# Optimization experiments

Hardware: AMD Instinct MI355X
Metric: run time of the kernel (lower is better)

Reference implementation:

```python
import jax, jax.numpy as jnp
import numpy as np

# dims matching init_kwargs / input_specs
N, C, H, W = 8, 256, 64, 64
OUT_C, KH, KW = 256, 3, 3
STRIDE, PAD = 1, 1
OUT_H = (H - KH + 2 * PAD) // STRIDE + 1  # 64
OUT_W = (W - KW + 2 * PAD) // STRIDE + 1  # 64
K = KH * KW


def setup_inputs() -> dict:
    key = jax.random.key(0)
    k1, k2, k3 = jax.random.split(key, 3)
    x = jax.random.normal(k1, (N, C, H, W), dtype=jnp.float32)
    offset = jax.random.normal(k2, (N, 2 * K, OUT_H, OUT_W), dtype=jnp.float32)
    # kaiming-uniform-ish scale for weight (fan_in = C*KH*KW)
    bound = 1.0 / np.sqrt(C * KH * KW)
    weight = jax.random.uniform(k3, (OUT_C, C, KH, KW), dtype=jnp.float32,
                                minval=-bound, maxval=bound)
    return {"input": x, "offset": offset, "weight": weight}


def _deform_conv(x, offset, weight):
    # base sampling positions in pixel coords: y = oy*stride + ky - pad
    ky = jnp.repeat(jnp.arange(KH, dtype=jnp.float32) - PAD, KW)  # [K]
    kx = jnp.tile(jnp.arange(KW, dtype=jnp.float32) - PAD, KH)    # [K]
    oy = jnp.arange(OUT_H, dtype=jnp.float32) * STRIDE            # [outH]
    ox = jnp.arange(OUT_W, dtype=jnp.float32) * STRIDE            # [outW]
    base_y = ky[:, None, None] + oy[None, :, None]  # [K, outH, 1]
    base_x = kx[:, None, None] + ox[None, None, :]  # [K, 1, outW]

    off = offset.reshape(N, K, 2, OUT_H, OUT_W)
    y = base_y[None] + off[:, :, 0]  # [N, K, outH, outW], offset channel 0 = dy
    xp = base_x[None] + off[:, :, 1]  # channel 1 = dx

    # bilinear sample with zero padding (grid_sample align_corners=True, zeros)
    y0 = jnp.floor(y)
    x0 = jnp.floor(xp)
    bidx = jnp.arange(N)[:, None, None, None]
    acc = jnp.zeros((N, K, OUT_H, OUT_W, C), dtype=x.dtype)
    for dy in (0.0, 1.0):
        for dx in (0.0, 1.0):
            yi = y0 + dy
            xi = x0 + dx
            wgt = (1.0 - jnp.abs(y - yi)) * (1.0 - jnp.abs(xp - xi))
            valid = ((yi >= 0) & (yi <= H - 1) & (xi >= 0) & (xi <= W - 1))
            yc = jnp.clip(yi, 0, H - 1).astype(jnp.int32)
            xc = jnp.clip(xi, 0, W - 1).astype(jnp.int32)
            g = x[bidx, :, yc, xc]  # [N, K, outH, outW, C]
            acc = acc + g * (wgt * valid.astype(x.dtype))[..., None]

    # weight.view(outC, -1) flattens (C, KH, KW) -> (C, K) ordering
    w = weight.reshape(OUT_C, C, K)
    out = jnp.einsum('nkhwc,ock->nohw', acc, w)  # [N, outC, outH, outW]
    return out


def reference(input, offset, weight):
    # NOTE: original forward never adds bias -> faithfully omitted
    return _deform_conv(input, offset, weight)
```

## Files before the change

### kernel.cpp

```cpp
#include <hip/hip_runtime.h>
#include <hip/hip_fp16.h>
#include <stdint.h>


typedef _Float16 half8 __attribute__((ext_vector_type(8)));
typedef float f32x4 __attribute__((ext_vector_type(4)));

__device__ __forceinline__ __half2 h2(uint32_t u) {
  return __builtin_bit_cast(__half2, u);
}
__device__ __forceinline__ uint32_t packh2f(float a, float b) {
  return __builtin_bit_cast(uint32_t, __floats2half2_rn(a, b));
}
__device__ __forceinline__ __half2 duplo(uint32_t u) {
  return __half2half2(__builtin_bit_cast(__half, (unsigned short)(u & 0xffffu)));
}
__device__ __forceinline__ __half2 duphi(uint32_t u) {
  return __half2half2(__builtin_bit_cast(__half, (unsigned short)(u >> 16)));
}

__global__ __launch_bounds__(256) void prep_all_kernel(
    const float* __restrict__ x, const float* __restrict__ w,
    const float* __restrict__ offset,
    unsigned short* __restrict__ xb, unsigned short* __restrict__ w3s,
    unsigned short* __restrict__ coords) {
  __shared__ float tile[64][65];
  int tid = threadIdx.x;
  if (blockIdx.x < 2048) {
    int bn   = blockIdx.x >> 8;
    int rem  = blockIdx.x & 255;
    int y    = rem >> 2;
    int cblk = rem & 3;
    const float* src = x + ((size_t)(bn * 256 + cblk * 64)) * 4096 + y * 64;
#pragma unroll
    for (int i = 0; i < 4; ++i) {
      int u  = i * 256 + tid;
      int cl = u >> 4;
      int xs = (u & 15) * 4;
      float4 v = *(const float4*)(src + cl * 4096 + xs);
      tile[cl][xs] = v.x; tile[cl][xs + 1] = v.y;
      tile[cl][xs + 2] = v.z; tile[cl][xs + 3] = v.w;
    }
    __syncthreads();
    unsigned short* dst = xb + ((size_t)(bn * 64 + y) * 64) * 256 + cblk * 64;
#pragma unroll
    for (int i = 0; i < 8; ++i) {
      int v2  = i * 256 + tid;
      int xc  = v2 >> 5;
      int cl2 = (v2 & 31) * 2;
      *(uint32_t*)(dst + xc * 256 + cl2) = packh2f(tile[cl2][xc], tile[cl2 + 1][xc]);
    }
  } else if (blockIdx.x < 4352) {
    int idx = (blockIdx.x - 2048) * 256 + tid;
    int t   = idx >> 14;
    int r2  = idx & 16383;
    int g   = r2 >> 3;
    int e   = r2 & 7;
    int oc  = g >> 3;
    int kk8 = (g & 7) ^ (oc & 7);
    int kk  = kk8 * 8 + e;
    int c   = (t & 3) * 64 + kk;
    int k   = t >> 2;
    w3s[idx] = __builtin_bit_cast(unsigned short, __float2half(w[(oc * 256 + c) * 9 + k]));
  } else {
    int idx = (blockIdx.x - 4352) * 256 + tid;
    int ow  = idx & 63;
    int oh  = (idx >> 6) & 63;
    int r   = idx >> 12;
    int k   = r % 9;
    int bn  = r / 9;
    int ky = k / 3 - 1;
    int kx = k % 3 - 1;
    float offy = offset[((bn * 18 + 2 * k    ) * 64 + oh) * 64 + ow];
    float offx = offset[((bn * 18 + 2 * k + 1) * 64 + oh) * 64 + ow];
    float y = (float)(oh + ky) + offy;
    float x2 = (float)(ow + kx) + offx;
    float y0f = floorf(y), x0f = floorf(x2);
    float fy = y - y0f, fx = x2 - x0f;
    int y0 = (int)y0f, x0 = (int)x0f;
    int y1 = y0 + 1, x1 = x0 + 1;
    float vy0 = (y0 >= 0 && y0 <= 63) ? 1.0f : 0.0f;
    float vy1 = (y1 >= 0 && y1 <= 63) ? 1.0f : 0.0f;
    float vx0 = (x0 >= 0 && x0 <= 63) ? 1.0f : 0.0f;
    float vx1 = (x1 >= 0 && x1 <= 63) ? 1.0f : 0.0f;
    float wy0 = (1.0f - fy) * vy0, wy1 = fy * vy1;
    float wx0 = (1.0f - fx) * vx0, wx1 = fx * vx1;
    int y0c = min(max(y0, 0), 63), y1c = min(max(y1, 0), 63);
    int x0c = min(max(x0, 0), 63), x1c = min(max(x1, 0), 63);
    unsigned short ent[8];
    ent[0] = __builtin_bit_cast(unsigned short, __float2half(wy0 * wx0));
    ent[1] = __builtin_bit_cast(unsigned short, __float2half(wy0 * wx1));
    ent[2] = __builtin_bit_cast(unsigned short, __float2half(wy1 * wx0));
    ent[3] = __builtin_bit_cast(unsigned short, __float2half(wy1 * wx1));
    ent[4] = (unsigned short)(y0c * 64 + x0c);
    ent[5] = (unsigned short)(y0c * 64 + x1c);
    ent[6] = (unsigned short)(y1c * 64 + x0c);
    ent[7] = (unsigned short)(y1c * 64 + x1c);
    *(uint4*)(coords + (size_t)idx * 8) = *(const uint4*)ent;
  }
}

__global__ __launch_bounds__(512, 4) void deform_mfma_kernel(
    const unsigned short* __restrict__ xb,
    const unsigned short* __restrict__ coords,
    const unsigned short* __restrict__ w3s,
    float* __restrict__ out) {
  __shared__ __align__(16) unsigned short At[64 * 72];
  __shared__ __align__(16) unsigned short Bt[256 * 64];

  int bn  = blockIdx.x & 7;
  int oh  = blockIdx.x >> 3;
  int tid = threadIdx.x;

  int w    = tid >> 6;
  int lane = tid & 63;
  int wrow = w & 1;
  int wcol = w >> 1;
  int mrow = lane & 15;
  int quad = lane >> 4;

  int srow = tid >> 3;
  int sg   = tid & 7;

  const unsigned short* xbn = xb + (size_t)bn * (64 * 64 * 256);
  const char* gbase = (const char*)xbn + sg * 16;
  const unsigned short* cbase = coords + ((size_t)((bn * 9) * 64 + oh) * 64 + srow) * 8;
  unsigned short* awr = At + srow * 72 + sg * 8;

  f32x4 acc[2][4] = {};

#define BDMA(TT)                                                                \
  {                                                                             \
    const unsigned short* src = w3s + (TT) * 16384;                             \
    _Pragma("unroll")                                                           \
    for (int j = 0; j < 4; ++j) {                                               \
      int base16 = j * 512 + w * 64;                                            \
      __builtin_amdgcn_global_load_lds(                                         \
          (const __attribute__((address_space(1))) void*)(src + (base16 + lane) * 8), \
          (__attribute__((address_space(3))) void*)(Bt + base16 * 8),           \
          16, 0, 0);                                                            \
    }                                                                           \
  }

#define ASTAGE(TT)                                                              \
  {                                                                             \
    uint4 c00 = *(const uint4*)(p00 + ((TT) & 3) * 128);                        \
    uint4 c01 = *(const uint4*)(p01 + ((TT) & 3) * 128);                        \
    uint4 c10 = *(const uint4*)(p10 + ((TT) & 3) * 128);                        \
    uint4 c11 = *(const uint4*)(p11 + ((TT) & 3) * 128);                        \
    __half2 r0 = __hmul2(h2(c00.x), w00);                                       \
    r0 = __hfma2(h2(c01.x), w01, r0);                                           \
    r0 = __hfma2(h2(c10.x), w10, r0);                                           \
    r0 = __hfma2(h2(c11.x), w11, r0);                                           \
    __half2 r1 = __hmul2(h2(c00.y), w00);                                       \
    r1 = __hfma2(h2(c01.y), w01, r1);                                           \
    r1 = __hfma2(h2(c10.y), w10, r1);                                           \
    r1 = __hfma2(h2(c11.y), w11, r1);                                           \
    __half2 r2 = __hmul2(h2(c00.z), w00);                                       \
    r2 = __hfma2(h2(c01.z), w01, r2);                                           \
    r2 = __hfma2(h2(c10.z), w10, r2);                                           \
    r2 = __hfma2(h2(c11.z), w11, r2);                                           \
    __half2 r3 = __hmul2(h2(c00.w), w00);                                       \
    r3 = __hfma2(h2(c01.w), w01, r3);                                           \
    r3 = __hfma2(h2(c10.w), w10, r3);                                           \
    r3 = __hfma2(h2(c11.w), w11, r3);                                           \
    uint4 pk;                                                                   \
    pk.x = __builtin_bit_cast(uint32_t, r0);                                    \
    pk.y = __builtin_bit_cast(uint32_t, r1);                                    \
    pk.z = __builtin_bit_cast(uint32_t, r2);                                    \
    pk.w = __builtin_bit_cast(uint32_t, r3);                                    \
    *(uint4*)awr = pk;                                                          \
  }

#define TAPSETUP(TAP)                                                           \
  {                                                                             \
    uint4 ce = *(const uint4*)(cbase + (TAP) * 32768);                          \
    w00 = duplo(ce.x); w01 = duphi(ce.x);                                       \
    w10 = duplo(ce.y); w11 = duphi(ce.y);                                       \
    p00 = gbase + ((size_t)(ce.z & 0xffffu) << 9);                              \
    p01 = gbase + ((size_t)(ce.z >> 16) << 9);                                  \
    p10 = gbase + ((size_t)(ce.w & 0xffffu) << 9);                              \
    p11 = gbase + ((size_t)(ce.w >> 16) << 9);                                  \
  }

  __half2 w00, w01, w10, w11;
  const char *p00, *p01, *p10, *p11;

  TAPSETUP(0)
  BDMA(0)
  ASTAGE(0)
  __syncthreads();

  half8 af[2][2];
  half8 bfr[2][4];

  for (int tap = 0; tap < 9; ++tap) {
#pragma unroll
    for (int cc = 0; cc < 4; ++cc) {
      const int t = tap * 4 + cc;
#pragma unroll
      for (int ks = 0; ks < 2; ++ks) {
#pragma unroll
        for (int m = 0; m < 2; ++m)
          af[m][ks] = *(const half8*)(&At[(wrow * 32 + m * 16 + mrow) * 72 + ks * 32 + quad * 8]);
#pragma unroll
        for (int nn = 0; nn < 4; ++nn) {
          int oc  = wcol * 64 + nn * 16 + mrow;
          int g16 = oc * 8 + ((ks * 4 + quad) ^ (mrow & 7));
          bfr[ks][nn] = *(const half8*)(&Bt[g16 * 8]);
        }
      }
      __syncthreads();

      if (t < 35) {
        BDMA(t + 1)
        if (cc == 3) TAPSETUP(tap + 1)
        ASTAGE(t + 1)
      }
#pragma unroll
      for (int ks = 0; ks < 2; ++ks)
#pragma unroll
        for (int m = 0; m < 2; ++m)
#pragma unroll
          for (int nn = 0; nn < 4; ++nn)
            acc[m][nn] = __builtin_amdgcn_mfma_f32_16x16x32_f16(af[m][ks], bfr[ks][nn], acc[m][nn], 0, 0, 0);
      __syncthreads();
    }
  }

  float* outp = out + (size_t)(bn * 256) * 4096 + oh * 64;
#pragma unroll
  for (int m = 0; m < 2; ++m) {
    int ow0 = wrow * 32 + m * 16 + quad * 4;
#pragma unroll
    for (int nn = 0; nn < 4; ++nn) {
      int oc = wcol * 64 + nn * 16 + mrow;
      *(f32x4*)(outp + oc * 4096 + ow0) = acc[m][nn];
    }
  }
#undef BDMA
#undef ASTAGE
#undef TAPSETUP
}

extern "C" void kernel_launch(void* const* d_in, const int* in_sizes, int n_in,
                              void* d_out, int out_size, void* d_ws, size_t ws_size,
                              hipStream_t stream) {
  (void)in_sizes; (void)n_in; (void)out_size; (void)ws_size;
  const float* x      = (const float*)d_in[0];
  const float* offset = (const float*)d_in[1];
  const float* weight = (const float*)d_in[2];
  float* out = (float*)d_out;

  unsigned short* xb     = (unsigned short*)d_ws;
  unsigned short* w3s    = xb + (size_t)8 * 64 * 64 * 256;
  unsigned short* coords = w3s + (size_t)36 * 16384;

  prep_all_kernel<<<5504, 256, 0, stream>>>(x, weight, offset, xb, w3s, coords);
  deform_mfma_kernel<<<512, 512, 0, stream>>>(xb, coords, w3s, out);
}
```

Baseline: 152.2 us.

## Double-buffer LDS A/B tiles and drop one barrier per k-step

Both the gathered-input tile and the weight tile in shared memory now have two buffers. The next stage's DMA and bilinear gather write into the other buffer while MFMA fragments are read from the current one, so one of the two __syncthreads per step goes away. The A tile drops its padded stride in favour of an XOR swizzle, and the coordinate entry for the next tap is fetched one stage ahead. The cost is roughly double the LDS footprint, which may reduce how many blocks fit on a CU.

```diff
diff --git a/kernel.cpp b/kernel.cpp
--- a/kernel.cpp
+++ b/kernel.cpp
@@ -105,8 +105,8 @@
     const unsigned short* __restrict__ coords,
     const unsigned short* __restrict__ w3s,
     float* __restrict__ out) {
-  __shared__ __align__(16) unsigned short At[64 * 72];
-  __shared__ __align__(16) unsigned short Bt[256 * 64];
+  __shared__ __align__(16) unsigned short At[2][64 * 64];
+  __shared__ __align__(16) unsigned short Bt[2][256 * 64];
 
   int bn  = blockIdx.x & 7;
   int oh  = blockIdx.x >> 3;
@@ -125,11 +125,13 @@
   const unsigned short* xbn = xb + (size_t)bn * (64 * 64 * 256);
   const char* gbase = (const char*)xbn + sg * 16;
   const unsigned short* cbase = coords + ((size_t)((bn * 9) * 64 + oh) * 64 + srow) * 8;
-  unsigned short* awr = At + srow * 72 + sg * 8;
+  int aw_off = srow * 64 + ((sg ^ (srow & 7)) * 8);
+  unsigned short* awr0 = &At[0][0] + aw_off;
+  unsigned short* awr1 = &At[1][0] + aw_off;
 
   f32x4 acc[2][4] = {};
 
-#define BDMA(TT)                                                                \
+#define BDMA(TT, BB)                                                            \
   {                                                                             \
     const unsigned short* src = w3s + (TT) * 16384;                             \
     _Pragma("unroll")                                                           \
@@ -137,12 +139,12 @@
       int base16 = j * 512 + w * 64;                                            \
       __builtin_amdgcn_global_load_lds(                                         \
           (const __attribute__((address_space(1))) void*)(src + (base16 + lane) * 8), \
-          (__attribute__((address_space(3))) void*)(Bt + base16 * 8),           \
+          (__attribute__((address_space(3))) void*)(&Bt[BB][0] + base16 * 8),   \
           16, 0, 0);                                                            \
     }                                                                           \
   }
 
-#define ASTAGE(TT)                                                              \
+#define ASTAGE(TT, AW)                                                          \
   {                                                                             \
     uint4 c00 = *(const uint4*)(p00 + ((TT) & 3) * 128);                        \
     uint4 c01 = *(const uint4*)(p01 + ((TT) & 3) * 128);                        \
@@ -169,26 +171,29 @@
     pk.y = __builtin_bit_cast(uint32_t, r1);                                    \
     pk.z = __builtin_bit_cast(uint32_t, r2);                                    \
     pk.w = __builtin_bit_cast(uint32_t, r3);                                    \
-    *(uint4*)awr = pk;                                                          \
-  }
-
-#define TAPSETUP(TAP)                                                           \
+    *(uint4*)(AW) = pk;                                                         \
+  }
+
+#define TAPSETUP_R(CE)                                                          \
   {                                                                             \
-    uint4 ce = *(const uint4*)(cbase + (TAP) * 32768);                          \
-    w00 = duplo(ce.x); w01 = duphi(ce.x);                                       \
-    w10 = duplo(ce.y); w11 = duphi(ce.y);                                       \
-    p00 = gbase + ((size_t)(ce.z & 0xffffu) << 9);                              \
-    p01 = gbase + ((size_t)(ce.z >> 16) << 9);                                  \
-    p10 = gbase + ((size_t)(ce.w & 0xffffu) << 9);                              \
-    p11 = gbase + ((size_t)(ce.w >> 16) << 9);                                  \
+    w00 = duplo((CE).x); w01 = duphi((CE).x);                                   \
+    w10 = duplo((CE).y); w11 = duphi((CE).y);                                   \
+    p00 = gbase + ((size_t)((CE).z & 0xffffu) << 9);                            \
+    p01 = gbase + ((size_t)((CE).z >> 16) << 9);                                \
+    p10 = gbase + ((size_t)((CE).w & 0xffffu) << 9);                            \
+    p11 = gbase + ((size_t)((CE).w >> 16) << 9);                                \
   }
 
   __half2 w00, w01, w10, w11;
   const char *p00, *p01, *p10, *p11;
-
-  TAPSETUP(0)
-  BDMA(0)
-  ASTAGE(0)
+  uint4 cnext;
+
+  {
+    uint4 ce0 = *(const uint4*)(cbase);
+    TAPSETUP_R(ce0)
+  }
+  BDMA(0, 0)
+  ASTAGE(0, awr0)
   __syncthreads();
 
   half8 af[2][2];
@@ -197,26 +202,35 @@
   for (int tap = 0; tap < 9; ++tap) {
 #pragma unroll
     for (int cc = 0; cc < 4; ++cc) {
-      const int t = tap * 4 + cc;
-#pragma unroll
-      for (int ks = 0; ks < 2; ++ks) {
-#pragma unroll
-        for (int m = 0; m < 2; ++m)
-          af[m][ks] = *(const half8*)(&At[(wrow * 32 + m * 16 + mrow) * 72 + ks * 32 + quad * 8]);
-#pragma unroll
-        for (int nn = 0; nn < 4; ++nn) {
-          int oc  = wcol * 64 + nn * 16 + mrow;
-          int g16 = oc * 8 + ((ks * 4 + quad) ^ (mrow & 7));
-          bfr[ks][nn] = *(const half8*)(&Bt[g16 * 8]);
+      const int t  = tap * 4 + cc;
+      const int pb = cc & 1;
+
+      if (t < 35) {
+        BDMA(t + 1, 1 - pb)
+        if (cc == 2 && tap < 8) cnext = *(const uint4*)(cbase + (tap + 1) * 32768);
+        if (cc == 3) TAPSETUP_R(cnext)
+        ASTAGE(t + 1, pb ? awr0 : awr1)
+      }
+
+      {
+        const unsigned short* Atp = &At[pb][0];
+        const unsigned short* Btp = &Bt[pb][0];
+#pragma unroll
+        for (int ks = 0; ks < 2; ++ks) {
+#pragma unroll
+          for (int m = 0; m < 2; ++m) {
+            int R = wrow * 32 + m * 16 + mrow;
+            af[m][ks] = *(const half8*)(Atp + R * 64 + (((ks * 4 + quad) ^ (mrow & 7)) * 8));
+          }
+#pragma unroll
+          for (int nn = 0; nn < 4; ++nn) {
+            int oc  = wcol * 64 + nn * 16 + mrow;
+            int g16 = oc * 8 + ((ks * 4 + quad) ^ (mrow & 7));
+            bfr[ks][nn] = *(const half8*)(Btp + g16 * 8);
+          }
         }
       }
-      __syncthreads();
-
-      if (t < 35) {
-        BDMA(t + 1)
-        if (cc == 3) TAPSETUP(tap + 1)
-        ASTAGE(t + 1)
-      }
+
 #pragma unroll
       for (int ks = 0; ks < 2; ++ks)
 #pragma unroll
@@ -224,6 +238,7 @@
 #pragma unroll
           for (int nn = 0; nn < 4; ++nn)
             acc[m][nn] = __builtin_amdgcn_mfma_f32_16x16x32_f16(af[m][ks], bfr[ks][nn], acc[m][nn], 0, 0, 0);
+
       __syncthreads();
     }
   }
@@ -240,7 +255,7 @@
   }
 #undef BDMA
 #undef ASTAGE
-#undef TAPSETUP
+#undef TAPSETUP_R
 }
 
 extern "C" void kernel_launch(void* const* d_in, const int* in_sizes, int n_in,
```

Result: faster. 147.1 us (-3.3%).

## Process two output rows per block with register-held weights and double-buffered LDS

Applied to the files above, without the earlier changes.

Each block now computes two output rows (128 pixels × 256 oc), halving the grid, so each wave covers 64 pixels × 64 oc with a 4×4 accumulator tile. Weight fragments are loaded straight from global memory into registers (alternating two register sets) instead of being staged in LDS with global_load_lds. The A tile is double-buffered in an XOR-swizzled LDS layout, so each stage needs one barrier instead of two. This raises register pressure (launch bounds drop to 2 blocks/CU) and puts repeated weight reads on the global/L2 path in exchange for more MFMA reuse per loaded fragment.

```diff
diff --git a/kernel.cpp b/kernel.cpp
--- a/kernel.cpp
+++ b/kernel.cpp
@@ -100,16 +100,15 @@
   }
 }
 
-__global__ __launch_bounds__(512, 4) void deform_mfma_kernel(
+__global__ __launch_bounds__(512, 2) void deform_mfma_kernel(
     const unsigned short* __restrict__ xb,
     const unsigned short* __restrict__ coords,
     const unsigned short* __restrict__ w3s,
     float* __restrict__ out) {
-  __shared__ __align__(16) unsigned short At[64 * 72];
-  __shared__ __align__(16) unsigned short Bt[256 * 64];
+  __shared__ __align__(16) unsigned short At[2][128 * 64];
 
   int bn  = blockIdx.x & 7;
-  int oh  = blockIdx.x >> 3;
+  int ohp = blockIdx.x >> 3;
   int tid = threadIdx.x;
 
   int w    = tid >> 6;
@@ -122,125 +121,158 @@
   int srow = tid >> 3;
   int sg   = tid & 7;
 
-  const unsigned short* xbn = xb + (size_t)bn * (64 * 64 * 256);
-  const char* gbase = (const char*)xbn + sg * 16;
-  const unsigned short* cbase = coords + ((size_t)((bn * 9) * 64 + oh) * 64 + srow) * 8;
-  unsigned short* awr = At + srow * 72 + sg * 8;
-
-  f32x4 acc[2][4] = {};
-
-#define BDMA(TT)                                                                \
-  {                                                                             \
-    const unsigned short* src = w3s + (TT) * 16384;                             \
+  const char* xbc = (const char*)(xb + (size_t)bn * (64 * 64 * 256));
+  const unsigned short* cb0 = coords + ((size_t)((bn * 9) * 64 + ohp * 2) * 64 + srow) * 8;
+  const unsigned short* cb1 = cb0 + 512;
+
+  int aw0 = srow * 64 + ((sg ^ (srow & 7)) * 8);
+  int grp0 = quad ^ (mrow & 7);
+  int grp1 = (4 + quad) ^ (mrow & 7);
+  int a_off0 = (wrow * 64 + mrow) * 64 + grp0 * 8;
+  int a_off1 = (wrow * 64 + mrow) * 64 + grp1 * 8;
+  int boff0 = ((wcol * 64 + mrow) * 8 + grp0) * 16;
+  int boff1 = ((wcol * 64 + mrow) * 8 + grp1) * 16;
+
+  f32x4 acc[4][4] = {};
+  half8 bA[2][4], bB[2][4];
+
+  __half2 w00, w01, w02, w03, w10, w11, w12, w13;
+  uint32_t o00, o01, o02, o03, o10, o11, o12, o13;
+  uint4 cn0, cn1;
+
+#define BLOADR(TT, BS)                                                          \
+  {                                                                             \
+    const char* wp = (const char*)w3s + (size_t)(TT) * 32768;                   \
     _Pragma("unroll")                                                           \
-    for (int j = 0; j < 4; ++j) {                                               \
-      int base16 = j * 512 + w * 64;                                            \
-      __builtin_amdgcn_global_load_lds(                                         \
-          (const __attribute__((address_space(1))) void*)(src + (base16 + lane) * 8), \
-          (__attribute__((address_space(3))) void*)(Bt + base16 * 8),           \
-          16, 0, 0);                                                            \
-    }                                                                           \
-  }
-
-#define ASTAGE(TT)                                                              \
-  {                                                                             \
-    uint4 c00 = *(const uint4*)(p00 + ((TT) & 3) * 128);                        \
-    uint4 c01 = *(const uint4*)(p01 + ((TT) & 3) * 128);                        \
-    uint4 c10 = *(const uint4*)(p10 + ((TT) & 3) * 128);                        \
-    uint4 c11 = *(const uint4*)(p11 + ((TT) & 3) * 128);                        \
-    __half2 r0 = __hmul2(h2(c00.x), w00);                                       \
-    r0 = __hfma2(h2(c01.x), w01, r0);                                           \
-    r0 = __hfma2(h2(c10.x), w10, r0);                                           \
-    r0 = __hfma2(h2(c11.x), w11, r0);                                           \
-    __half2 r1 = __hmul2(h2(c00.y), w00);                                       \
-    r1 = __hfma2(h2(c01.y), w01, r1);                                           \
-    r1 = __hfma2(h2(c10.y), w10, r1);                                           \
-    r1 = __hfma2(h2(c11.y), w11, r1);                                           \
-    __half2 r2 = __hmul2(h2(c00.z), w00);                                       \
-    r2 = __hfma2(h2(c01.z), w01, r2);                                           \
-    r2 = __hfma2(h2(c10.z), w10, r2);                                           \
-    r2 = __hfma2(h2(c11.z), w11, r2);                                           \
-    __half2 r3 = __hmul2(h2(c00.w), w00);                                       \
-    r3 = __hfma2(h2(c01.w), w01, r3);                                           \
-    r3 = __hfma2(h2(c10.w), w10, r3);                                           \
-    r3 = __hfma2(h2(c11.w), w11, r3);                                           \
-    uint4 pk;                                                                   \
-    pk.x = __builtin_bit_cast(uint32_t, r0);                                    \
-    pk.y = __builtin_bit_cast(uint32_t, r1);                                    \
-    pk.z = __builtin_bit_cast(uint32_t, r2);                                    \
-    pk.w = __builtin_bit_cast(uint32_t, r3);                                    \
-    *(uint4*)awr = pk;                                                          \
-  }
-
-#define TAPSETUP(TAP)                                                           \
-  {                                                                             \
-    uint4 ce = *(const uint4*)(cbase + (TAP) * 32768);                          \
-    w00 = duplo(ce.x); w01 = duphi(ce.x);                                       \
-    w10 = duplo(ce.y); w11 = duphi(ce.y);                                       \
-    p00 = gbase + ((size_t)(ce.z & 0xffffu) << 9);                              \
-    p01 = gbase + ((size_t)(ce.z >> 16) << 9);                                  \
-    p10 = gbase + ((size_t)(ce.w & 0xffffu) << 9);                              \
-    p11 = gbase + ((size_t)(ce.w >> 16) << 9);                                  \
-  }
-
-  __half2 w00, w01, w10, w11;
-  const char *p00, *p01, *p10, *p11;
-
-  TAPSETUP(0)
-  BDMA(0)
-  ASTAGE(0)
+    for (int nn = 0; nn < 4; ++nn) {                                            \
+      BS[0][nn] = *(const half8*)(wp + boff0 + nn * 2048);                      \
+      BS[1][nn] = *(const half8*)(wp + boff1 + nn * 2048);                      \
+    }                                                                           \
+  }
+
+#define TAPSETUP_R(CE0, CE1)                                                    \
+  {                                                                             \
+    w00 = duplo((CE0).x); w01 = duphi((CE0).x);                                 \
+    w02 = duplo((CE0).y); w03 = duphi((CE0).y);                                 \
+    o00 = (((CE0).z & 0xffffu) << 9) + sg * 16;                                 \
+    o01 = (((CE0).z >> 16) << 9) + sg * 16;                                     \
+    o02 = (((CE0).w & 0xffffu) << 9) + sg * 16;                                 \
+    o03 = (((CE0).w >> 16) << 9) + sg * 16;                                     \
+    w10 = duplo((CE1).x); w11 = duphi((CE1).x);                                 \
+    w12 = duplo((CE1).y); w13 = duphi((CE1).y);                                 \
+    o10 = (((CE1).z & 0xffffu) << 9) + sg * 16;                                 \
+    o11 = (((CE1).z >> 16) << 9) + sg * 16;                                     \
+    o12 = (((CE1).w & 0xffffu) << 9) + sg * 16;                                 \
+    o13 = (((CE1).w >> 16) << 9) + sg * 16;                                     \
+  }
+
+#define ASTAGE(TT, ATP)                                                         \
+  {                                                                             \
+    {                                                                           \
+      uint4 c0 = *(const uint4*)(xbc + o00 + ((TT) & 3) * 128);                 \
+      uint4 c1 = *(const uint4*)(xbc + o01 + ((TT) & 3) * 128);                 \
+      uint4 c2 = *(const uint4*)(xbc + o02 + ((TT) & 3) * 128);                 \
+      uint4 c3 = *(const uint4*)(xbc + o03 + ((TT) & 3) * 128);                 \
+      __half2 r0 = __hmul2(h2(c0.x), w00);                                      \
+      r0 = __hfma2(h2(c1.x), w01, r0); r0 = __hfma2(h2(c2.x), w02, r0);         \
+      r0 = __hfma2(h2(c3.x), w03, r0);                                          \
+      __half2 r1 = __hmul2(h2(c0.y), w00);                                      \
+      r1 = __hfma2(h2(c1.y), w01, r1); r1 = __hfma2(h2(c2.y), w02, r1);         \
+      r1 = __hfma2(h2(c3.y), w03, r1);                                          \
+      __half2 r2 = __hmul2(h2(c0.z), w00);                                      \
+      r2 = __hfma2(h2(c1.z), w01, r2); r2 = __hfma2(h2(c2.z), w02, r2);         \
+      r2 = __hfma2(h2(c3.z), w03, r2);                                          \
+      __half2 r3 = __hmul2(h2(c0.w), w00);                                      \
+      r3 = __hfma2(h2(c1.w), w01, r3); r3 = __hfma2(h2(c2.w), w02, r3);         \
+      r3 = __hfma2(h2(c3.w), w03, r3);                                          \
+      uint4 pk;                                                                 \
+      pk.x = __builtin_bit_cast(uint32_t, r0);                                  \
+      pk.y = __builtin_bit_cast(uint32_t, r1);                                  \
+      pk.z = __builtin_bit_cast(uint32_t, r2);                                  \
+      pk.w = __builtin_bit_cast(uint32_t, r3);                                  \
+      *(uint4*)((ATP) + aw0) = pk;                                              \
+    }                                                                           \
+    {                                                                           \
+      uint4 c0 = *(const uint4*)(xbc + o10 + ((TT) & 3) * 128);                 \
+      uint4 c1 = *(const uint4*)(xbc + o11 + ((TT) & 3) * 128);                 \
+      uint4 c2 = *(const uint4*)(xbc + o12 + ((TT) & 3) * 128);                 \
+      uint4 c3 = *(const uint4*)(xbc + o13 + ((TT) & 3) * 128);                 \
+      __half2 r0 = __hmul2(h2(c0.x), w10);                                      \
+      r0 = __hfma2(h2(c1.x), w11, r0); r0 = __hfma2(h2(c2.x), w12, r0);         \
+      r0 = __hfma2(h2(c3.x), w13, r0);                                          \
+      __half2 r1 = __hmul2(h2(c0.y), w10);                                      \
+      r1 = __hfma2(h2(c1.y), w11, r1); r1 = __hfma2(h2(c2.y), w12, r1);         \
+      r1 = __hfma2(h2(c3.y), w13, r1);                                          \
+      __half2 r2 = __hmul2(h2(c0.z), w10);                                      \
+      r2 = __hfma2(h2(c1.z), w11, r2); r2 = __hfma2(h2(c2.z), w12, r2);         \
+      r2 = __hfma2(h2(c3.z), w13, r2);                                          \
+      __half2 r3 = __hmul2(h2(c0.w), w10);                                      \
+      r3 = __hfma2(h2(c1.w), w11, r3); r3 = __hfma2(h2(c2.w), w12, r3);         \
+      r3 = __hfma2(h2(c3.w), w13, r3);                                          \
+      uint4 pk;                                                                 \
+      pk.x = __builtin_bit_cast(uint32_t, r0);                                  \
+      pk.y = __builtin_bit_cast(uint32_t, r1);                                  \
+      pk.z = __builtin_bit_cast(uint32_t, r2);                                  \
+      pk.w = __builtin_bit_cast(uint32_t, r3);                                  \
+      *(uint4*)((ATP) + aw0 + 4096) = pk;                                       \
+    }                                                                           \
+  }
+
+#define COMPUTE(ATP, BS)                                                        \
+  {                                                                             \
+    _Pragma("unroll")                                                           \
+    for (int m = 0; m < 4; ++m) {                                               \
+      half8 af0 = *(const half8*)((ATP) + a_off0 + m * 1024);                   \
+      half8 af1 = *(const half8*)((ATP) + a_off1 + m * 1024);                   \
+      _Pragma("unroll")                                                         \
+      for (int nn = 0; nn < 4; ++nn) {                                          \
+        acc[m][nn] = __builtin_amdgcn_mfma_f32_16x16x32_f16(af0, BS[0][nn], acc[m][nn], 0, 0, 0); \
+        acc[m][nn] = __builtin_amdgcn_mfma_f32_16x16x32_f16(af1, BS[1][nn], acc[m][nn], 0, 0, 0); \
+      }                                                                         \
+    }                                                                           \
+  }
+
+  {
+    uint4 ce0 = *(const uint4*)cb0;
+    uint4 ce1 = *(const uint4*)cb1;
+    TAPSETUP_R(ce0, ce1)
+  }
+  BLOADR(0, bA)
+  ASTAGE(0, &At[0][0])
   __syncthreads();
-
-  half8 af[2][2];
-  half8 bfr[2][4];
 
   for (int tap = 0; tap < 9; ++tap) {
 #pragma unroll
     for (int cc = 0; cc < 4; ++cc) {
       const int t = tap * 4 + cc;
-#pragma unroll
-      for (int ks = 0; ks < 2; ++ks) {
-#pragma unroll
-        for (int m = 0; m < 2; ++m)
-          af[m][ks] = *(const half8*)(&At[(wrow * 32 + m * 16 + mrow) * 72 + ks * 32 + quad * 8]);
-#pragma unroll
-        for (int nn = 0; nn < 4; ++nn) {
-          int oc  = wcol * 64 + nn * 16 + mrow;
-          int g16 = oc * 8 + ((ks * 4 + quad) ^ (mrow & 7));
-          bfr[ks][nn] = *(const half8*)(&Bt[g16 * 8]);
+      if (t < 35) {
+        if (cc & 1) { BLOADR(t + 1, bA) } else { BLOADR(t + 1, bB) }
+        if (cc == 2 && tap < 8) {
+          cn0 = *(const uint4*)(cb0 + (tap + 1) * 32768);
+          cn1 = *(const uint4*)(cb1 + (tap + 1) * 32768);
         }
+        if (cc == 3) TAPSETUP_R(cn0, cn1)
+        if (cc & 1) { ASTAGE(t + 1, &At[0][0]) } else { ASTAGE(t + 1, &At[1][0]) }
       }
+      if (cc & 1) { COMPUTE(&At[1][0], bB) } else { COMPUTE(&At[0][0], bA) }
       __syncthreads();
-
-      if (t < 35) {
-        BDMA(t + 1)
-        if (cc == 3) TAPSETUP(tap + 1)
-        ASTAGE(t + 1)
-      }
-#pragma unroll
-      for (int ks = 0; ks < 2; ++ks)
-#pragma unroll
-        for (int m = 0; m < 2; ++m)
-#pragma unroll
-          for (int nn = 0; nn < 4; ++nn)
-            acc[m][nn] = __builtin_amdgcn_mfma_f32_16x16x32_f16(af[m][ks], bfr[ks][nn], acc[m][nn], 0, 0, 0);
-      __syncthreads();
-    }
-  }
-
-  float* outp = out + (size_t)(bn * 256) * 4096 + oh * 64;
-#pragma unroll
-  for (int m = 0; m < 2; ++m) {
-    int ow0 = wrow * 32 + m * 16 + quad * 4;
+    }
+  }
+
+  float* outp = out + (size_t)bn * 256 * 4096 + (size_t)(ohp * 2 + wrow) * 64;
+#pragma unroll
+  for (int m = 0; m < 4; ++m) {
+    int ow0 = m * 16 + quad * 4;
 #pragma unroll
     for (int nn = 0; nn < 4; ++nn) {
       int oc = wcol * 64 + nn * 16 + mrow;
-      *(f32x4*)(outp + oc * 4096 + ow0) = acc[m][nn];
-    }
-  }
-#undef BDMA
+      *(f32x4*)(outp + (size_t)oc * 4096 + ow0) = acc[m][nn];
+    }
+  }
+#undef BLOADR
+#undef TAPSETUP_R
 #undef ASTAGE
-#undef TAPSETUP
+#undef COMPUTE
 }
 
 extern "C" void kernel_launch(void* const* d_in, const int* in_sizes, int n_in,
@@ -257,5 +289,5 @@
   unsigned short* coords = w3s + (size_t)36 * 16384;
 
   prep_all_kernel<<<5504, 256, 0, stream>>>(x, weight, offset, xb, w3s, coords);
-  deform_mfma_kernel<<<512, 512, 0, stream>>>(xb, coords, w3s, out);
-}
+  deform_mfma_kernel<<<256, 512, 0, stream>>>(xb, coords, w3s, out);
+}
```

Measured after the change: 144.8 us. 1.05x faster.
